# Kernel tuning notes

Measured on AMD Instinct MI355X. Metric: run time of the kernel, lower is better.

## Reference

```python
import jax, jax.numpy as jnp
import numpy as np

D_MODEL = 1024
NUM_HEADS = 16
SEQ_LEN = 2048
WINDOW_SIZES = (5, 10, 20, 40)


def _avg_gaussian_mask(seq_len, dtype=jnp.float32):
    # mask[i,j] = exp(-(i-j)^2/(2 w^2)) if j <= i else 0; averaged over 4 windows.
    i = jnp.arange(seq_len, dtype=dtype)[:, None]
    j = jnp.arange(seq_len, dtype=dtype)[None, :]
    d2 = (i - j) ** 2
    lower = (j <= i)
    masks = [jnp.where(lower, jnp.exp(-d2 / (2.0 * w * w)), 0.0) for w in WINDOW_SIZES]
    return sum(masks) / len(WINDOW_SIZES)  # [S, S]


def setup_inputs() -> dict:
    key = jax.random.key(0)
    ks = jax.random.split(key, 11)
    B, S, D = 2, SEQ_LEN, D_MODEL
    std = 1.0 / np.sqrt(D)
    inp = {
        "Q": jax.random.normal(ks[0], (B, S, D), jnp.float32),
        "K": jax.random.normal(ks[1], (B, S, D), jnp.float32),
        "V": jax.random.normal(ks[2], (B, S, D), jnp.float32),
        "Wq": jax.random.uniform(ks[3], (D, D), jnp.float32, -std, std),
        "bq": jax.random.uniform(ks[4], (D,), jnp.float32, -std, std),
        "Wk": jax.random.uniform(ks[5], (D, D), jnp.float32, -std, std),
        "bk": jax.random.uniform(ks[6], (D,), jnp.float32, -std, std),
        "Wv": jax.random.uniform(ks[7], (D, D), jnp.float32, -std, std),
        "bv": jax.random.uniform(ks[8], (D,), jnp.float32, -std, std),
        "Wo": jax.random.uniform(ks[9], (D, D), jnp.float32, -std, std),
        "bo": jax.random.uniform(ks[10], (D,), jnp.float32, -std, std),
    }
    return inp


def reference(Q, K, V, Wq, bq, Wk, bk, Wv, bv, Wo, bo):
    B, S, D = Q.shape
    H, dk = NUM_HEADS, D // NUM_HEADS

    def proj(x, W, b):
        # torch Linear: x @ W^T + b, then split heads -> [B, H, S, dk]
        y = x @ W.T + b
        return y.reshape(B, S, H, dk).transpose(0, 2, 1, 3)

    q = proj(Q, Wq, bq)
    k = proj(K, Wk, bk)
    v = proj(V, Wv, bv)

    # mean over mask dim of (scores + mask_m) == scores + mean(mask)
    avg_mask = _avg_gaussian_mask(S, q.dtype)  # [S, S]
    scores = jnp.einsum('bhqd,bhkd->bhqk', q, k) / jnp.sqrt(jnp.asarray(dk, q.dtype))
    scores = scores + avg_mask  # broadcast over [B, H]
    probs = jax.nn.softmax(scores, axis=-1)
    out = jnp.einsum('bhqk,bhkd->bhqd', probs, v)
    out = out.transpose(0, 2, 1, 3).reshape(B, S, D)
    return out @ Wo.T + bo
```

## Files before the change

### kernel.cpp

```cpp
#include <hip/hip_runtime.h>
#include <hip/hip_bf16.h>


#define S_LEN 2048
#define D_MODEL 1024
#define NHEADS 16
#define DK 64
#define BATCH 2
#define M_ROWS (BATCH * S_LEN)
#define LOG2E 1.4426950408889634f

typedef float f32x4 __attribute__((ext_vector_type(4)));
typedef short s16x8 __attribute__((ext_vector_type(8)));
typedef unsigned short u16x4 __attribute__((ext_vector_type(4)));
typedef unsigned u32x2 __attribute__((ext_vector_type(2)));

__device__ __forceinline__ unsigned short f2bf(float f) {
    unsigned u = __builtin_bit_cast(unsigned, f);
    u = (u + 0x7FFFu + ((u >> 16) & 1u)) >> 16;
    return (unsigned short)u;
}

__device__ __forceinline__ float fast_exp2(float x) {
    float r;
    asm("v_exp_f32 %0, %1" : "=v"(r) : "v"(x));
    return r;
}

__device__ __forceinline__ unsigned cvt_pk_bf16(float a, float b) {
    unsigned r;
    asm("v_cvt_pk_bf16_f32 %0, %1, %2" : "=v"(r) : "v"(a), "v"(b));
    return r;
}

__device__ __forceinline__ float max3f(float a, float b, float c) {
    float r;
    asm("v_max3_f32 %0, %1, %2, %3" : "=v"(r) : "v"(a), "v"(b), "v"(c));
    return r;
}

#define GLD16(gptr, lptr)                                                     \
    __builtin_amdgcn_global_load_lds(                                         \
        (const __attribute__((address_space(1))) void*)(gptr),                \
        (__attribute__((address_space(3))) void*)(lptr), 16, 0, 0)

__global__ void mask_kernel(float* __restrict__ mtab) {
    int d = blockIdx.x * 256 + threadIdx.x;
    if (d < S_LEN) {
        float d2 = (float)d * (float)d;
        mtab[d] = LOG2E * 0.25f * (__expf(-d2 * (1.0f / 50.0f)) +
                                   __expf(-d2 * (1.0f / 200.0f)) +
                                   __expf(-d2 * (1.0f / 800.0f)) +
                                   __expf(-d2 * (1.0f / 3200.0f)));
    }
}

__global__ __launch_bounds__(256) void convert_kernel(
    const float* __restrict__ Q, const float* __restrict__ K,
    const float* __restrict__ V,
    const float* __restrict__ Wq, const float* __restrict__ Wk,
    const float* __restrict__ Wv, const float* __restrict__ Wo,
    unsigned short* __restrict__ Qb, unsigned short* __restrict__ Kb,
    unsigned short* __restrict__ Vb,
    unsigned short* __restrict__ Wqb, unsigned short* __restrict__ Wkb,
    unsigned short* __restrict__ Wvb, unsigned short* __restrict__ Wob)
{
    const int XN = M_ROWS * D_MODEL / 8;
    const int WN = D_MODEL * D_MODEL / 8;
    int i = blockIdx.x * 256 + threadIdx.x;
    const float* src;
    unsigned short* dst;
    int off;
    if (i < 3 * XN) {
        if (i < XN)          { src = Q; dst = Qb; off = i; }
        else if (i < 2 * XN) { src = K; dst = Kb; off = i - XN; }
        else                 { src = V; dst = Vb; off = i - 2 * XN; }
    } else {
        int j = i - 3 * XN;
        if (j < WN)          { src = Wq; dst = Wqb; off = j; }
        else if (j < 2 * WN) { src = Wk; dst = Wkb; off = j - WN; }
        else if (j < 3 * WN) { src = Wv; dst = Wvb; off = j - 2 * WN; }
        else                 { src = Wo; dst = Wob; off = j - 3 * WN; }
    }
    f32x4 v0 = *(const f32x4*)(src + (size_t)off * 8);
    f32x4 v1 = *(const f32x4*)(src + (size_t)off * 8 + 4);
    s16x8 o;
#pragma unroll
    for (int j = 0; j < 4; ++j) {
        o[j]     = (short)f2bf(v0[j]);
        o[j + 4] = (short)f2bf(v1[j]);
    }
    *(s16x8*)(dst + (size_t)off * 8) = o;
}

__device__ __forceinline__ void gemm_core_128(
    const unsigned short* __restrict__ A, const unsigned short* __restrict__ B,
    unsigned short* As, unsigned short* Bs,
    int m0, int n0, int K, int tid, f32x4 acc[4][4])
{
    const int wid  = tid >> 6;
    const int lane = tid & 63;
    const int g    = lane >> 4;
    const int c    = lane & 15;
    const int wm   = wid >> 1;
    const int wn   = wid & 1;

    const int srow   = tid >> 3;
    const int schunk = tid & 7;

    for (int kt = 0; kt < K / 64; ++kt) {
        const int k0 = kt * 64;
        __syncthreads();
#pragma unroll
        for (int r = 0; r < 4; ++r) {
            const int row = r * 32 + srow;
            GLD16(A + (size_t)(m0 + row) * K + k0 + schunk * 8,
                  &As[(r * 256 + wid * 64) * 8]);
        }
#pragma unroll
        for (int r = 0; r < 4; ++r) {
            const int row = r * 32 + srow;
            GLD16(B + (size_t)(n0 + row) * K + k0 + schunk * 8,
                  &Bs[(r * 256 + wid * 64) * 8]);
        }
        __syncthreads();

        s16x8 a[2][4];
#pragma unroll
        for (int ks = 0; ks < 2; ++ks)
#pragma unroll
            for (int mf = 0; mf < 4; ++mf)
                a[ks][mf] = *(const s16x8*)
                    &As[(wm * 64 + mf * 16 + c) * 64 + ks * 32 + g * 8];
#pragma unroll
        for (int ks = 0; ks < 2; ++ks) {
#pragma unroll
            for (int nf = 0; nf < 4; ++nf) {
                s16x8 b = *(const s16x8*)
                    &Bs[(wn * 64 + nf * 16 + c) * 64 + ks * 32 + g * 8];
#pragma unroll
                for (int mf = 0; mf < 4; ++mf)
                    acc[mf][nf] = __builtin_amdgcn_mfma_f32_16x16x32_bf16(
                        a[ks][mf], b, acc[mf][nf], 0, 0, 0);
            }
        }
    }
}

__global__ __launch_bounds__(256) void proj_gemm(
    const unsigned short* __restrict__ Qx, const unsigned short* __restrict__ Kx,
    const unsigned short* __restrict__ Vx,
    const unsigned short* __restrict__ Wq, const unsigned short* __restrict__ Wk,
    const unsigned short* __restrict__ Wv,
    const float* __restrict__ bq, const float* __restrict__ bk,
    const float* __restrict__ bv,
    unsigned short* __restrict__ qo, unsigned short* __restrict__ ko,
    unsigned short* __restrict__ vo)
{
    const int z = blockIdx.z;
    const unsigned short* X = (z == 0) ? Qx : (z == 1) ? Kx : Vx;
    const unsigned short* W = (z == 0) ? Wq : (z == 1) ? Wk : Wv;
    const float* bias       = (z == 0) ? bq : (z == 1) ? bk : bv;
    unsigned short* out     = (z == 0) ? qo : (z == 1) ? ko : vo;
    const float scale = (z == 0) ? (0.125f * LOG2E) : 1.0f;

    __shared__ unsigned short As[128 * 64];
    __shared__ unsigned short Bs[128 * 64];

    const int tid = threadIdx.x;
    const int m0  = blockIdx.x * 128;
    const int n0  = blockIdx.y * 128;

    f32x4 acc[4][4];
#pragma unroll
    for (int i = 0; i < 4; ++i)
#pragma unroll
        for (int j = 0; j < 4; ++j) acc[i][j] = (f32x4){0.f, 0.f, 0.f, 0.f};

    gemm_core_128(X, W, As, Bs, m0, n0, D_MODEL, tid, acc);

    const int lane = tid & 63;
    const int g    = lane >> 4;
    const int c    = lane & 15;
    const int wm   = (tid >> 6) >> 1;
    const int wn   = (tid >> 6) & 1;

#pragma unroll
    for (int mf = 0; mf < 4; ++mf) {
#pragma unroll
        for (int nf = 0; nf < 4; ++nf) {
            const int o = n0 + wn * 64 + nf * 16 + c;
            const float bv_ = bias[o];
            const int h  = o >> 6;
            const int dd = o & 63;
#pragma unroll
            for (int r = 0; r < 4; ++r) {
                const int m = m0 + wm * 64 + mf * 16 + g * 4 + r;
                const int b = m >> 11;
                const int s = m & (S_LEN - 1);
                const float val = (acc[mf][nf][r] + bv_) * scale;
                out[(((size_t)(b * NHEADS + h)) * S_LEN + s) * DK + dd] = f2bf(val);
            }
        }
    }
}

__global__ __launch_bounds__(256) void out_gemm(
    const unsigned short* __restrict__ A,
    const unsigned short* __restrict__ W,
    const float* __restrict__ bias,
    float* __restrict__ out)
{
    __shared__ unsigned short As[128 * 64];
    __shared__ unsigned short Bs[128 * 64];

    const int tid = threadIdx.x;
    const int m0  = blockIdx.x * 128;
    const int n0  = blockIdx.y * 128;

    f32x4 acc[4][4];
#pragma unroll
    for (int i = 0; i < 4; ++i)
#pragma unroll
        for (int j = 0; j < 4; ++j) acc[i][j] = (f32x4){0.f, 0.f, 0.f, 0.f};

    gemm_core_128(A, W, As, Bs, m0, n0, D_MODEL, tid, acc);

    const int lane = tid & 63;
    const int g    = lane >> 4;
    const int c    = lane & 15;
    const int wm   = (tid >> 6) >> 1;
    const int wn   = (tid >> 6) & 1;

#pragma unroll
    for (int mf = 0; mf < 4; ++mf) {
#pragma unroll
        for (int nf = 0; nf < 4; ++nf) {
            const int o = n0 + wn * 64 + nf * 16 + c;
            const float bv_ = bias[o];
#pragma unroll
            for (int r = 0; r < 4; ++r) {
                const int m = m0 + wm * 64 + mf * 16 + g * 4 + r;
                out[(size_t)m * D_MODEL + o] = acc[mf][nf][r] + bv_;
            }
        }
    }
}

#define VSWZ(row) ((((row) >> 1) & 7) << 4)

__global__ __launch_bounds__(512) void attn_kernel(
    const unsigned short* __restrict__ qh,
    const unsigned short* __restrict__ kh,
    const unsigned short* __restrict__ vh,
    const float* __restrict__ mask_tab,
    unsigned short* __restrict__ attn_out)
{
    __shared__ float mtab[S_LEN];
    __shared__ unsigned short Kt[64 * 64];
    __shared__ unsigned short Vt[64 * 64];
    __shared__ unsigned short Pt[8][16 * 64];

    const int tid  = threadIdx.x;
    const int wid  = tid >> 6;
    const int lane = tid & 63;
    const int g    = lane >> 4;
    const int c    = lane & 15;
    const int bh   = blockIdx.y;
    const int b    = bh >> 4;
    const int h    = bh & 15;
    const int q0w  = blockIdx.x * 128 + wid * 16;

    *(f32x4*)&mtab[tid * 4] = *(const f32x4*)&mask_tab[tid * 4];

    const size_t head_off = (size_t)bh * S_LEN * DK;
    const unsigned short* qp = qh + head_off;
    const unsigned short* kp = kh + head_off;
    const unsigned short* vp = vh + head_off;

    s16x8 aq[2];
    {
        const unsigned short* qrow = qp + (size_t)(q0w + c) * DK;
        aq[0] = *(const s16x8*)(qrow + g * 8);
        aq[1] = *(const s16x8*)(qrow + 32 + g * 8);
    }

    f32x4 acc_o[4];
#pragma unroll
    for (int nf = 0; nf < 4; ++nf) acc_o[nf] = (f32x4){0.f, 0.f, 0.f, 0.f};
    float m_l = -1e30f, l_l = 0.f;

    const int srowK = tid >> 3;
    const int soffE = (tid & 7) * 8;
    const int vd0   = (tid & 31) * 2;
    const int vkq   = (tid >> 5) * 4;

    s16x8 kreg;
    unsigned vreg[4];
    kreg = *(const s16x8*)&kp[(size_t)srowK * DK + soffE];
#pragma unroll
    for (int i = 0; i < 4; ++i)
        vreg[i] = *(const unsigned*)&vp[(size_t)(vkq + i) * DK + vd0];

    unsigned short* Ptw = Pt[wid];

    for (int kt = 0; kt < S_LEN / 64; ++kt) {
        const int k0 = kt * 64;
        __syncthreads();

        *(s16x8*)((char*)Kt + srowK * 128 + ((soffE * 2) ^ ((srowK & 7) << 4))) = kreg;
        {
            u16x4 lo4, hi4;
#pragma unroll
            for (int i = 0; i < 4; ++i) {
                lo4[i] = (unsigned short)vreg[i];
                hi4[i] = (unsigned short)(vreg[i] >> 16);
            }
            *(u16x4*)((char*)Vt + vd0 * 128 + ((vkq * 2) ^ VSWZ(vd0))) = lo4;
            *(u16x4*)((char*)Vt + (vd0 + 1) * 128 +
                      ((vkq * 2) ^ VSWZ(vd0 + 1))) = hi4;
        }
        if (kt < S_LEN / 64 - 1) {
            const int k1 = k0 + 64;
            kreg = *(const s16x8*)&kp[(size_t)(k1 + srowK) * DK + soffE];
#pragma unroll
            for (int i = 0; i < 4; ++i)
                vreg[i] = *(const unsigned*)&vp[(size_t)(k1 + vkq + i) * DK + vd0];
        }
        __syncthreads();

        f32x4 st[4];
        __builtin_amdgcn_s_setprio(1);
#pragma unroll
        for (int nf = 0; nf < 4; ++nf) {
            st[nf] = (f32x4){0.f, 0.f, 0.f, 0.f};
#pragma unroll
            for (int f = 0; f < 2; ++f) {
                const int row = nf * 16 + c;
                s16x8 kf = *(const s16x8*)((const char*)Kt + row * 128 +
                                           ((f * 64 + g * 16) ^ ((row & 7) << 4)));
                st[nf] = __builtin_amdgcn_mfma_f32_16x16x32_bf16(
                    kf, aq[f], st[nf], 0, 0, 0);
            }
        }
        __builtin_amdgcn_s_setprio(0);

        const int diff = q0w - k0;
        if (diff >= -15 && diff <= 510) {
            const int dbase = q0w + c - k0;
#pragma unroll
            for (int nf = 0; nf < 4; ++nf) {
#pragma unroll
                for (int r = 0; r < 4; ++r) {
                    const int d = dbase - (nf * 16 + g * 4 + r);
                    if (d >= 0) st[nf][r] += mtab[d];
                }
            }
        }

        float tm = st[0][0];
        tm = max3f(tm, st[0][1], st[0][2]);
        tm = max3f(tm, st[0][3], st[1][0]);
        tm = max3f(tm, st[1][1], st[1][2]);
        tm = max3f(tm, st[1][3], st[2][0]);
        tm = max3f(tm, st[2][1], st[2][2]);
        tm = max3f(tm, st[2][3], st[3][0]);
        tm = max3f(tm, st[3][1], st[3][2]);
        tm = fmaxf(tm, st[3][3]);
        tm = fmaxf(tm, __shfl_xor(tm, 16));
        tm = fmaxf(tm, __shfl_xor(tm, 32));

        if (__any(tm > m_l + 8.0f)) {
            const float mnew = fmaxf(m_l, tm);
            const float csc  = fast_exp2(m_l - mnew);
            m_l = mnew;
            l_l *= csc;
            f32x4 cscv;
#pragma unroll
            for (int r = 0; r < 4; ++r) cscv[r] = __shfl(csc, g * 4 + r);
#pragma unroll
            for (int nf = 0; nf < 4; ++nf) acc_o[nf] *= cscv;
        }

#pragma unroll
        for (int nf = 0; nf < 4; ++nf)
#pragma unroll
            for (int r = 0; r < 4; ++r)
                st[nf][r] = fast_exp2(st[nf][r] - m_l);
        {
            f32x4 s4 = (st[0] + st[1]) + (st[2] + st[3]);
            float ps = (s4[0] + s4[1]) + (s4[2] + s4[3]);
            ps += __shfl_xor(ps, 16);
            ps += __shfl_xor(ps, 32);
            l_l += ps;
        }

#pragma unroll
        for (int nf = 0; nf < 4; ++nf) {
            u32x2 pk;
            pk[0] = cvt_pk_bf16(st[nf][0], st[nf][1]);
            pk[1] = cvt_pk_bf16(st[nf][2], st[nf][3]);
            *(u32x2*)((char*)Ptw + c * 128 +
                      ((nf * 32 + g * 8) ^ ((c & 7) << 4))) = pk;
        }

        __builtin_amdgcn_s_setprio(1);
#pragma unroll
        for (int f = 0; f < 2; ++f) {
            s16x8 pa = *(const s16x8*)((const char*)Ptw + c * 128 +
                                       ((f * 64 + g * 16) ^ ((c & 7) << 4)));
#pragma unroll
            for (int nf = 0; nf < 4; ++nf) {
                const int row = nf * 16 + c;
                s16x8 vb = *(const s16x8*)((const char*)Vt + row * 128 +
                                           ((f * 64 + g * 16) ^ VSWZ(row)));
                acc_o[nf] = __builtin_amdgcn_mfma_f32_16x16x32_bf16(
                    pa, vb, acc_o[nf], 0, 0, 0);
            }
        }
        __builtin_amdgcn_s_setprio(0);
    }

    float lq[4];
#pragma unroll
    for (int r = 0; r < 4; ++r) lq[r] = __shfl(l_l, g * 4 + r);
#pragma unroll
    for (int nf = 0; nf < 4; ++nf) {
#pragma unroll
        for (int r = 0; r < 4; ++r) {
            const int i_glob = q0w + g * 4 + r;
            const int d = nf * 16 + c;
            const float o = acc_o[nf][r] / lq[r];
            attn_out[((size_t)(b * S_LEN + i_glob)) * D_MODEL + h * DK + d] = f2bf(o);
        }
    }
}

extern "C" void kernel_launch(void* const* d_in, const int* in_sizes, int n_in,
                              void* d_out, int out_size, void* d_ws, size_t ws_size,
                              hipStream_t stream) {
    const float* Q  = (const float*)d_in[0];
    const float* K  = (const float*)d_in[1];
    const float* V  = (const float*)d_in[2];
    const float* Wq = (const float*)d_in[3];
    const float* bq = (const float*)d_in[4];
    const float* Wk = (const float*)d_in[5];
    const float* bk = (const float*)d_in[6];
    const float* Wv = (const float*)d_in[7];
    const float* bv = (const float*)d_in[8];
    const float* Wo = (const float*)d_in[9];
    const float* bo = (const float*)d_in[10];
    float* out = (float*)d_out;

    const size_t XE = (size_t)M_ROWS * D_MODEL;
    const size_t WE = (size_t)D_MODEL * D_MODEL;
    unsigned short* qh  = (unsigned short*)d_ws;
    unsigned short* kh  = qh + XE;
    unsigned short* vh  = kh + XE;
    unsigned short* ah  = vh + XE;
    unsigned short* Qb  = ah + XE;
    unsigned short* Kb  = Qb + XE;
    unsigned short* Vb  = Kb + XE;
    unsigned short* Wqb = Vb + XE;
    unsigned short* Wkb = Wqb + WE;
    unsigned short* Wvb = Wkb + WE;
    unsigned short* Wob = Wvb + WE;
    float* mtab = (float*)(Wob + WE);

    mask_kernel<<<dim3(S_LEN / 256), 256, 0, stream>>>(mtab);
    convert_kernel<<<dim3((3 * XE / 8 + 4 * WE / 8) / 256), 256, 0, stream>>>(
        Q, K, V, Wq, Wk, Wv, Wo, Qb, Kb, Vb, Wqb, Wkb, Wvb, Wob);
    proj_gemm<<<dim3(M_ROWS / 128, D_MODEL / 128, 3), 256, 0, stream>>>(
        Qb, Kb, Vb, Wqb, Wkb, Wvb, bq, bk, bv, qh, kh, vh);
    attn_kernel<<<dim3(S_LEN / 128, BATCH * NHEADS), 512, 0, stream>>>(
        qh, kh, vh, mtab, ah);
    out_gemm<<<dim3(M_ROWS / 128, D_MODEL / 128), 256, 0, stream>>>(
        ah, Wob, bo, out);
}
```

Before: 153.0 us.

## Restructure attention to 2 waves with 32 query rows each, padded LDS, block swizzle

Result: slower. 163.9 us (+7.1%).

```diff
diff --git a/kernel.cpp b/kernel.cpp
--- a/kernel.cpp
+++ b/kernel.cpp
@@ -9,10 +9,11 @@
 #define BATCH 2
 #define M_ROWS (BATCH * S_LEN)
 #define LOG2E 1.4426950408889634f
+#define LSTR 72
 
 typedef float f32x4 __attribute__((ext_vector_type(4)));
 typedef short s16x8 __attribute__((ext_vector_type(8)));
-typedef unsigned short u16x4 __attribute__((ext_vector_type(4)));
+typedef unsigned short u16x8 __attribute__((ext_vector_type(8)));
 typedef unsigned u32x2 __attribute__((ext_vector_type(2)));
 
 __device__ __forceinline__ unsigned short f2bf(float f) {
@@ -168,8 +169,10 @@
     __shared__ unsigned short Bs[128 * 64];
 
     const int tid = threadIdx.x;
-    const int m0  = blockIdx.x * 128;
-    const int n0  = blockIdx.y * 128;
+    const int flat = blockIdx.y * 32 + blockIdx.x;
+    const int sw   = (flat & 7) * 32 + (flat >> 3);
+    const int m0   = (sw & 31) * 128;
+    const int n0   = (sw >> 5) * 128;
 
     f32x4 acc[4][4];
 #pragma unroll
@@ -215,8 +218,10 @@
     __shared__ unsigned short Bs[128 * 64];
 
     const int tid = threadIdx.x;
-    const int m0  = blockIdx.x * 128;
-    const int n0  = blockIdx.y * 128;
+    const int flat = blockIdx.y * 32 + blockIdx.x;
+    const int sw   = (flat & 7) * 32 + (flat >> 3);
+    const int m0   = (sw & 31) * 128;
+    const int n0   = (sw >> 5) * 128;
 
     f32x4 acc[4][4];
 #pragma unroll
@@ -247,9 +252,7 @@
     }
 }
 
-#define VSWZ(row) ((((row) >> 1) & 7) << 4)
-
-__global__ __launch_bounds__(512) void attn_kernel(
+__global__ __launch_bounds__(128) void attn_kernel(
     const unsigned short* __restrict__ qh,
     const unsigned short* __restrict__ kh,
     const unsigned short* __restrict__ vh,
@@ -257,50 +260,64 @@
     unsigned short* __restrict__ attn_out)
 {
     __shared__ float mtab[S_LEN];
-    __shared__ unsigned short Kt[64 * 64];
-    __shared__ unsigned short Vt[64 * 64];
-    __shared__ unsigned short Pt[8][16 * 64];
+    __shared__ unsigned short Kt[64 * LSTR];
+    __shared__ unsigned short Vt[64 * LSTR];
+    __shared__ unsigned short Pt[2][32 * LSTR];
 
     const int tid  = threadIdx.x;
     const int wid  = tid >> 6;
     const int lane = tid & 63;
     const int g    = lane >> 4;
     const int c    = lane & 15;
-    const int bh   = blockIdx.y;
+
+    const int flat = blockIdx.y * 32 + blockIdx.x;
+    const int sw   = (flat & 7) * 128 + (flat >> 3);
+    const int bh   = sw >> 5;
+    const int bx   = sw & 31;
     const int b    = bh >> 4;
     const int h    = bh & 15;
-    const int q0w  = blockIdx.x * 128 + wid * 16;
-
-    *(f32x4*)&mtab[tid * 4] = *(const f32x4*)&mask_tab[tid * 4];
+    const int q0w  = bx * 64 + wid * 32;
+
+#pragma unroll
+    for (int i = 0; i < 4; ++i)
+        *(f32x4*)&mtab[tid * 16 + i * 4] = *(const f32x4*)&mask_tab[tid * 16 + i * 4];
 
     const size_t head_off = (size_t)bh * S_LEN * DK;
     const unsigned short* qp = qh + head_off;
     const unsigned short* kp = kh + head_off;
     const unsigned short* vp = vh + head_off;
 
-    s16x8 aq[2];
-    {
-        const unsigned short* qrow = qp + (size_t)(q0w + c) * DK;
-        aq[0] = *(const s16x8*)(qrow + g * 8);
-        aq[1] = *(const s16x8*)(qrow + 32 + g * 8);
-    }
-
-    f32x4 acc_o[4];
-#pragma unroll
-    for (int nf = 0; nf < 4; ++nf) acc_o[nf] = (f32x4){0.f, 0.f, 0.f, 0.f};
-    float m_l = -1e30f, l_l = 0.f;
-
-    const int srowK = tid >> 3;
-    const int soffE = (tid & 7) * 8;
-    const int vd0   = (tid & 31) * 2;
-    const int vkq   = (tid >> 5) * 4;
-
-    s16x8 kreg;
-    unsigned vreg[4];
-    kreg = *(const s16x8*)&kp[(size_t)srowK * DK + soffE];
+    s16x8 aq[2][2];
+#pragma unroll
+    for (int qf = 0; qf < 2; ++qf) {
+        const unsigned short* qrow = qp + (size_t)(q0w + qf * 16 + c) * DK;
+        aq[qf][0] = *(const s16x8*)(qrow + g * 8);
+        aq[qf][1] = *(const s16x8*)(qrow + 32 + g * 8);
+    }
+
+    f32x4 acc_o[2][4];
+#pragma unroll
+    for (int qf = 0; qf < 2; ++qf)
+#pragma unroll
+        for (int nf = 0; nf < 4; ++nf) acc_o[qf][nf] = (f32x4){0.f, 0.f, 0.f, 0.f};
+    float m_l[2] = {-1e30f, -1e30f};
+    f32x4 lsum[2];
+    lsum[0] = (f32x4){0.f, 0.f, 0.f, 0.f};
+    lsum[1] = (f32x4){0.f, 0.f, 0.f, 0.f};
+
+    const int krow = tid >> 1;
+    const int kcol = (tid & 1) * 32;
+    const int vd0  = (tid & 31) * 2;
+    const int vk16 = (tid >> 5) * 16;
+
+    s16x8 kreg[4];
+    unsigned vreg[16];
 #pragma unroll
     for (int i = 0; i < 4; ++i)
-        vreg[i] = *(const unsigned*)&vp[(size_t)(vkq + i) * DK + vd0];
+        kreg[i] = *(const s16x8*)&kp[(size_t)krow * DK + kcol + i * 8];
+#pragma unroll
+    for (int i = 0; i < 16; ++i)
+        vreg[i] = *(const unsigned*)&vp[(size_t)(vk16 + i) * DK + vd0];
 
     unsigned short* Ptw = Pt[wid];
 
@@ -308,130 +325,154 @@
         const int k0 = kt * 64;
         __syncthreads();
 
-        *(s16x8*)((char*)Kt + srowK * 128 + ((soffE * 2) ^ ((srowK & 7) << 4))) = kreg;
+#pragma unroll
+        for (int i = 0; i < 4; ++i)
+            *(s16x8*)&Kt[krow * LSTR + kcol + i * 8] = kreg[i];
         {
-            u16x4 lo4, hi4;
-#pragma unroll
-            for (int i = 0; i < 4; ++i) {
-                lo4[i] = (unsigned short)vreg[i];
-                hi4[i] = (unsigned short)(vreg[i] >> 16);
-            }
-            *(u16x4*)((char*)Vt + vd0 * 128 + ((vkq * 2) ^ VSWZ(vd0))) = lo4;
-            *(u16x4*)((char*)Vt + (vd0 + 1) * 128 +
-                      ((vkq * 2) ^ VSWZ(vd0 + 1))) = hi4;
+            u16x8 p0, p1, p2, p3;
+#pragma unroll
+            for (int i = 0; i < 8; ++i) {
+                p0[i] = (unsigned short)vreg[i];
+                p1[i] = (unsigned short)vreg[8 + i];
+                p2[i] = (unsigned short)(vreg[i] >> 16);
+                p3[i] = (unsigned short)(vreg[8 + i] >> 16);
+            }
+            *(u16x8*)&Vt[vd0 * LSTR + vk16]           = p0;
+            *(u16x8*)&Vt[vd0 * LSTR + vk16 + 8]       = p1;
+            *(u16x8*)&Vt[(vd0 + 1) * LSTR + vk16]     = p2;
+            *(u16x8*)&Vt[(vd0 + 1) * LSTR + vk16 + 8] = p3;
         }
         if (kt < S_LEN / 64 - 1) {
             const int k1 = k0 + 64;
-            kreg = *(const s16x8*)&kp[(size_t)(k1 + srowK) * DK + soffE];
 #pragma unroll
             for (int i = 0; i < 4; ++i)
-                vreg[i] = *(const unsigned*)&vp[(size_t)(k1 + vkq + i) * DK + vd0];
+                kreg[i] = *(const s16x8*)&kp[(size_t)(k1 + krow) * DK + kcol + i * 8];
+#pragma unroll
+            for (int i = 0; i < 16; ++i)
+                vreg[i] = *(const unsigned*)&vp[(size_t)(k1 + vk16 + i) * DK + vd0];
         }
         __syncthreads();
 
-        f32x4 st[4];
+        f32x4 st[2][4];
         __builtin_amdgcn_s_setprio(1);
 #pragma unroll
         for (int nf = 0; nf < 4; ++nf) {
-            st[nf] = (f32x4){0.f, 0.f, 0.f, 0.f};
-#pragma unroll
-            for (int f = 0; f < 2; ++f) {
-                const int row = nf * 16 + c;
-                s16x8 kf = *(const s16x8*)((const char*)Kt + row * 128 +
-                                           ((f * 64 + g * 16) ^ ((row & 7) << 4)));
-                st[nf] = __builtin_amdgcn_mfma_f32_16x16x32_bf16(
-                    kf, aq[f], st[nf], 0, 0, 0);
-            }
+            const unsigned short* kr = &Kt[(nf * 16 + c) * LSTR + g * 8];
+            s16x8 kf0 = *(const s16x8*)kr;
+            s16x8 kf1 = *(const s16x8*)(kr + 32);
+            st[0][nf] = __builtin_amdgcn_mfma_f32_16x16x32_bf16(
+                kf0, aq[0][0], (f32x4){0.f, 0.f, 0.f, 0.f}, 0, 0, 0);
+            st[0][nf] = __builtin_amdgcn_mfma_f32_16x16x32_bf16(
+                kf1, aq[0][1], st[0][nf], 0, 0, 0);
+            st[1][nf] = __builtin_amdgcn_mfma_f32_16x16x32_bf16(
+                kf0, aq[1][0], (f32x4){0.f, 0.f, 0.f, 0.f}, 0, 0, 0);
+            st[1][nf] = __builtin_amdgcn_mfma_f32_16x16x32_bf16(
+                kf1, aq[1][1], st[1][nf], 0, 0, 0);
         }
         __builtin_amdgcn_s_setprio(0);
 
         const int diff = q0w - k0;
-        if (diff >= -15 && diff <= 510) {
-            const int dbase = q0w + c - k0;
+        if (diff >= -31 && diff <= 510) {
+#pragma unroll
+            for (int qf = 0; qf < 2; ++qf) {
+                const int dbase = q0w + qf * 16 + c - k0;
+#pragma unroll
+                for (int nf = 0; nf < 4; ++nf)
+#pragma unroll
+                    for (int r = 0; r < 4; ++r) {
+                        const int d = dbase - (nf * 16 + g * 4 + r);
+                        if (d >= 0) st[qf][nf][r] += mtab[d];
+                    }
+            }
+        }
+
+        float tm[2];
+#pragma unroll
+        for (int qf = 0; qf < 2; ++qf) {
+            float t = max3f(st[qf][0][0], st[qf][0][1], st[qf][0][2]);
+            t = max3f(t, st[qf][0][3], st[qf][1][0]);
+            t = max3f(t, st[qf][1][1], st[qf][1][2]);
+            t = max3f(t, st[qf][1][3], st[qf][2][0]);
+            t = max3f(t, st[qf][2][1], st[qf][2][2]);
+            t = max3f(t, st[qf][2][3], st[qf][3][0]);
+            t = max3f(t, st[qf][3][1], st[qf][3][2]);
+            tm[qf] = fmaxf(t, st[qf][3][3]);
+        }
+
+        if (__any(tm[0] > m_l[0] + 8.0f || tm[1] > m_l[1] + 8.0f)) {
+#pragma unroll
+            for (int qf = 0; qf < 2; ++qf) {
+                float t = tm[qf];
+                t = fmaxf(t, __shfl_xor(t, 16));
+                t = fmaxf(t, __shfl_xor(t, 32));
+                const float mnew = fmaxf(m_l[qf], t);
+                const float csc  = fast_exp2(m_l[qf] - mnew);
+                m_l[qf] = mnew;
+                lsum[qf] *= csc;
+                f32x4 cscv;
+#pragma unroll
+                for (int r = 0; r < 4; ++r) cscv[r] = __shfl(csc, g * 4 + r);
+#pragma unroll
+                for (int nf = 0; nf < 4; ++nf) acc_o[qf][nf] *= cscv;
+            }
+        }
+
+#pragma unroll
+        for (int qf = 0; qf < 2; ++qf) {
+#pragma unroll
+            for (int nf = 0; nf < 4; ++nf)
+#pragma unroll
+                for (int r = 0; r < 4; ++r)
+                    st[qf][nf][r] = fast_exp2(st[qf][nf][r] - m_l[qf]);
+            lsum[qf] += (st[qf][0] + st[qf][1]) + (st[qf][2] + st[qf][3]);
 #pragma unroll
             for (int nf = 0; nf < 4; ++nf) {
-#pragma unroll
-                for (int r = 0; r < 4; ++r) {
-                    const int d = dbase - (nf * 16 + g * 4 + r);
-                    if (d >= 0) st[nf][r] += mtab[d];
-                }
-            }
-        }
-
-        float tm = st[0][0];
-        tm = max3f(tm, st[0][1], st[0][2]);
-        tm = max3f(tm, st[0][3], st[1][0]);
-        tm = max3f(tm, st[1][1], st[1][2]);
-        tm = max3f(tm, st[1][3], st[2][0]);
-        tm = max3f(tm, st[2][1], st[2][2]);
-        tm = max3f(tm, st[2][3], st[3][0]);
-        tm = max3f(tm, st[3][1], st[3][2]);
-        tm = fmaxf(tm, st[3][3]);
-        tm = fmaxf(tm, __shfl_xor(tm, 16));
-        tm = fmaxf(tm, __shfl_xor(tm, 32));
-
-        if (__any(tm > m_l + 8.0f)) {
-            const float mnew = fmaxf(m_l, tm);
-            const float csc  = fast_exp2(m_l - mnew);
-            m_l = mnew;
-            l_l *= csc;
-            f32x4 cscv;
-#pragma unroll
-            for (int r = 0; r < 4; ++r) cscv[r] = __shfl(csc, g * 4 + r);
-#pragma unroll
-            for (int nf = 0; nf < 4; ++nf) acc_o[nf] *= cscv;
-        }
-
-#pragma unroll
-        for (int nf = 0; nf < 4; ++nf)
-#pragma unroll
-            for (int r = 0; r < 4; ++r)
-                st[nf][r] = fast_exp2(st[nf][r] - m_l);
-        {
-            f32x4 s4 = (st[0] + st[1]) + (st[2] + st[3]);
-            float ps = (s4[0] + s4[1]) + (s4[2] + s4[3]);
-            ps += __shfl_xor(ps, 16);
-            ps += __shfl_xor(ps, 32);
-            l_l += ps;
-        }
-
+                u32x2 pk;
+                pk[0] = cvt_pk_bf16(st[qf][nf][0], st[qf][nf][1]);
+                pk[1] = cvt_pk_bf16(st[qf][nf][2], st[qf][nf][3]);
+                *(u32x2*)&Ptw[(qf * 16 + c) * LSTR + nf * 16 + g * 4] = pk;
+            }
+        }
+
+        __builtin_amdgcn_s_setprio(1);
+#pragma unroll
+        for (int f = 0; f < 2; ++f) {
+            s16x8 pa0 = *(const s16x8*)&Ptw[c * LSTR + f * 32 + g * 8];
+            s16x8 pa1 = *(const s16x8*)&Ptw[(16 + c) * LSTR + f * 32 + g * 8];
+#pragma unroll
+            for (int nf = 0; nf < 4; ++nf) {
+                s16x8 vb = *(const s16x8*)&Vt[(nf * 16 + c) * LSTR + f * 32 + g * 8];
+                acc_o[0][nf] = __builtin_amdgcn_mfma_f32_16x16x32_bf16(
+                    pa0, vb, acc_o[0][nf], 0, 0, 0);
+                acc_o[1][nf] = __builtin_amdgcn_mfma_f32_16x16x32_bf16(
+                    pa1, vb, acc_o[1][nf], 0, 0, 0);
+            }
+        }
+        __builtin_amdgcn_s_setprio(0);
+    }
+
+    float lq[2];
+#pragma unroll
+    for (int qf = 0; qf < 2; ++qf) {
+        float l = (lsum[qf][0] + lsum[qf][1]) + (lsum[qf][2] + lsum[qf][3]);
+        l += __shfl_xor(l, 16);
+        l += __shfl_xor(l, 32);
+        lq[qf] = l;
+    }
+#pragma unroll
+    for (int qf = 0; qf < 2; ++qf) {
+        f32x4 linv;
+#pragma unroll
+        for (int r = 0; r < 4; ++r) linv[r] = 1.0f / __shfl(lq[qf], g * 4 + r);
 #pragma unroll
         for (int nf = 0; nf < 4; ++nf) {
-            u32x2 pk;
-            pk[0] = cvt_pk_bf16(st[nf][0], st[nf][1]);
-            pk[1] = cvt_pk_bf16(st[nf][2], st[nf][3]);
-            *(u32x2*)((char*)Ptw + c * 128 +
-                      ((nf * 32 + g * 8) ^ ((c & 7) << 4))) = pk;
-        }
-
-        __builtin_amdgcn_s_setprio(1);
-#pragma unroll
-        for (int f = 0; f < 2; ++f) {
-            s16x8 pa = *(const s16x8*)((const char*)Ptw + c * 128 +
-                                       ((f * 64 + g * 16) ^ ((c & 7) << 4)));
-#pragma unroll
-            for (int nf = 0; nf < 4; ++nf) {
-                const int row = nf * 16 + c;
-                s16x8 vb = *(const s16x8*)((const char*)Vt + row * 128 +
-                                           ((f * 64 + g * 16) ^ VSWZ(row)));
-                acc_o[nf] = __builtin_amdgcn_mfma_f32_16x16x32_bf16(
-                    pa, vb, acc_o[nf], 0, 0, 0);
-            }
-        }
-        __builtin_amdgcn_s_setprio(0);
-    }
-
-    float lq[4];
-#pragma unroll
-    for (int r = 0; r < 4; ++r) lq[r] = __shfl(l_l, g * 4 + r);
-#pragma unroll
-    for (int nf = 0; nf < 4; ++nf) {
-#pragma unroll
-        for (int r = 0; r < 4; ++r) {
-            const int i_glob = q0w + g * 4 + r;
-            const int d = nf * 16 + c;
-            const float o = acc_o[nf][r] / lq[r];
-            attn_out[((size_t)(b * S_LEN + i_glob)) * D_MODEL + h * DK + d] = f2bf(o);
+#pragma unroll
+            for (int r = 0; r < 4; ++r) {
+                const int i_glob = q0w + qf * 16 + g * 4 + r;
+                const int d = nf * 16 + c;
+                attn_out[((size_t)(b * S_LEN + i_glob)) * D_MODEL + h * DK + d] =
+                    f2bf(acc_o[qf][nf][r] * linv[r]);
+            }
         }
     }
 }
@@ -470,10 +511,10 @@
     mask_kernel<<<dim3(S_LEN / 256), 256, 0, stream>>>(mtab);
     convert_kernel<<<dim3((3 * XE / 8 + 4 * WE / 8) / 256), 256, 0, stream>>>(
         Q, K, V, Wq, Wk, Wv, Wo, Qb, Kb, Vb, Wqb, Wkb, Wvb, Wob);
-    proj_gemm<<<dim3(M_ROWS / 128, D_MODEL / 128, 3), 256, 0, stream>>>(
+    proj_gemm<<<dim3(32, 8, 3), 256, 0, stream>>>(
         Qb, Kb, Vb, Wqb, Wkb, Wvb, bq, bk, bv, qh, kh, vh);
-    attn_kernel<<<dim3(S_LEN / 128, BATCH * NHEADS), 512, 0, stream>>>(
+    attn_kernel<<<dim3(32, 32), 128, 0, stream>>>(
         qh, kh, vh, mtab, ah);
-    out_gemm<<<dim3(M_ROWS / 128, D_MODEL / 128), 256, 0, stream>>>(
+    out_gemm<<<dim3(32, 8), 256, 0, stream>>>(
         ah, Wob, bo, out);
 }
```
